# Performance work log

Measured on AMD Instinct MI355X. Metric: run time of the kernel, lower is better.

Reference implementation:

```python
import jax, jax.numpy as jnp
import numpy as np

N_QUBITS = 10
DEPTH = 5
NUM_CLASSES = 2
DIM = 2 ** N_QUBITS  # 1024


def _rx(t):
    # RX(t) = [[cos(t/2), -i sin(t/2)], [-i sin(t/2), cos(t/2)]]
    c, s = jnp.cos(t / 2), jnp.sin(t / 2)
    zr = jnp.zeros_like(t)
    a = jax.lax.complex(c, zr)
    b = jax.lax.complex(zr, -s)
    return jnp.stack([jnp.stack([a, b]), jnp.stack([b, a])]).astype(jnp.complex64)


def _rz(t):
    # RZ(t) = diag(e^{-it/2}, e^{it/2})
    c, s = jnp.cos(t / 2), jnp.sin(t / 2)
    e = jax.lax.complex(c, -s)
    z = jnp.zeros_like(e)
    return jnp.stack([jnp.stack([e, z]), jnp.stack([z, jnp.conj(e)])]).astype(jnp.complex64)


def _apply_1q(state, U, wire):
    # state: (B, 2, ..., 2); wire axis is wire+1 (wire 0 = most significant bit)
    s = jnp.moveaxis(state, wire + 1, -1)
    s = s @ U.T
    return jnp.moveaxis(s, -1, wire + 1)


def _apply_c1q(state, U, ctrl, tgt):
    # controlled-U: apply U on tgt where ctrl qubit is |1>
    s = jnp.moveaxis(state, ctrl + 1, 1)  # (B, 2_ctrl, rest...)
    ax = tgt + 1 if tgt < ctrl else tgt   # tgt axis inside s[:, k]
    s1 = s[:, 1]
    s1 = jnp.moveaxis(s1, ax, -1) @ U.T
    s1 = jnp.moveaxis(s1, -1, ax)
    s = jnp.stack([s[:, 0], s1], axis=1)
    return jnp.moveaxis(s, 1, ctrl + 1)


def _circuit(x, weights, weights_1, weights_2):
    B = x.shape[0]
    x = x.reshape(B, -1)
    x = jnp.pad(x, ((0, 0), (0, DIM - x.shape[1])))  # pad_with=0
    x = x / jnp.linalg.norm(x, axis=1, keepdims=True)  # normalize=True
    state = jax.lax.complex(x, jnp.zeros_like(x)).reshape((B,) + (2,) * N_QUBITS)
    for d in range(DEPTH):
        for i in range(N_QUBITS):
            state = _apply_1q(state, _rx(weights[d, i, 0]), i)
            state = _apply_1q(state, _rz(weights[d, i, 1]), i)
            state = _apply_1q(state, _rx(weights[d, i, 2]), i)
        r = 1 if d % 2 == 0 else 3  # alternating entangler range (CCQC)
        for i in range(N_QUBITS):
            c = (i + r) % N_QUBITS
            state = _apply_c1q(state, _rz(weights[d, i, 3]), c, i)
            state = _apply_c1q(state, _rx(weights[d, i, 4]), c, i)
        state = _apply_1q(state, _rx(weights_1[d]), 0)
        state = _apply_1q(state, _rz(weights_2[d]), 0)
    probs = (jnp.abs(state) ** 2).reshape(B, DIM)
    # <Z_w> signs: bit w (MSB-first) of each basis index
    bits = (jnp.arange(DIM)[None, :] >> (N_QUBITS - 1 - jnp.arange(N_QUBITS)[:, None])) & 1
    zsign = (1 - 2 * bits).astype(probs.dtype)  # (n_qubits, DIM)
    return probs @ zsign.T  # (B, n_qubits)


def setup_inputs() -> dict:
    key = jax.random.key(0)
    ks = jax.random.split(key, 5)
    B = 8192
    x = jax.random.normal(ks[0], (B, 784), dtype=jnp.float32)
    y = jax.random.randint(ks[1], (B,), 0, NUM_CLASSES)
    weights = jax.random.uniform(ks[2], (DEPTH, N_QUBITS, 5), jnp.float32, 0.0, 2 * np.pi)
    weights_1 = jax.random.uniform(ks[3], (DEPTH,), jnp.float32, 0.0, 2 * np.pi)
    weights_2 = jax.random.uniform(ks[4], (DEPTH,), jnp.float32, 0.0, 2 * np.pi)
    return {"x": x, "y": y, "weights": weights, "weights_1": weights_1, "weights_2": weights_2}


def reference(x, y, weights, weights_1, weights_2):
    expz = _circuit(x, weights, weights_1, weights_2)
    logits = expz[:, :NUM_CLASSES]
    logp = jax.nn.log_softmax(logits, axis=-1)
    nll = -jnp.take_along_axis(logp, y[:, None].astype(jnp.int32), axis=1)[:, 0]
    return jnp.mean(nll)  # CrossEntropyLoss (mean reduction)
```

## Files before the change

kernel.cpp:

```cpp
#include <hip/hip_runtime.h>


namespace {

typedef float f32x2 __attribute__((ext_vector_type(2)));
typedef __fp16 fp16x2 __attribute__((ext_vector_type(2)));
typedef _Float16 f16x8 __attribute__((ext_vector_type(8)));
typedef float f32x4v __attribute__((ext_vector_type(4)));

__device__ __forceinline__ f32x2 pk_mul(f32x2 a, f32x2 b) {
  f32x2 d;
  asm("v_pk_mul_f32 %0, %1, %2" : "=v"(d) : "v"(a), "v"(b));
  return d;
}
__device__ __forceinline__ f32x2 pk_fma(f32x2 a, f32x2 b, f32x2 c) {
  f32x2 d;
  asm("v_pk_fma_f32 %0, %1, %2, %3" : "=v"(d) : "v"(a), "v"(b), "v"(c));
  return d;
}
__device__ __forceinline__ f32x2 pk_fma_swap1(f32x2 a, f32x2 b, f32x2 c) {
  f32x2 d;
  asm("v_pk_fma_f32 %0, %1, %2, %3 op_sel:[0,1,0] op_sel_hi:[1,0,1]"
      : "=v"(d) : "v"(a), "v"(b), "v"(c));
  return d;
}
__device__ __forceinline__ f32x2 cmulp(f32x2 cr2, f32x2 ci2, f32x2 v) {
  return pk_fma_swap1(ci2, v, pk_mul(cr2, v));
}
__device__ __forceinline__ f32x2 cmad(f32x2 acc, f32x2 cr2, f32x2 ci2, f32x2 v) {
  return pk_fma_swap1(ci2, v, pk_fma(cr2, v, acc));
}

__device__ __forceinline__ f32x2 shfl_xor2(f32x2 v, int lm) {
  f32x2 r;
  r.x = __shfl_xor(v.x, lm, 64);
  r.y = __shfl_xor(v.y, lm, 64);
  return r;
}
template <int CTRL>
__device__ __forceinline__ f32x2 dpp_xor2(f32x2 v) {
  f32x2 r;
  const int ix = __builtin_bit_cast(int, v.x);
  const int iy = __builtin_bit_cast(int, v.y);
  r.x = __builtin_bit_cast(float,
      __builtin_amdgcn_update_dpp(0, ix, CTRL, 0xF, 0xF, true));
  r.y = __builtin_bit_cast(float,
      __builtin_amdgcn_update_dpp(0, iy, CTRL, 0xF, 0xF, true));
  return r;
}
__device__ __forceinline__ f32x2 shfl_fast(f32x2 v, const int lm) {
  if (lm == 1) return dpp_xor2<0xB1>(v);
  if (lm == 2) return dpp_xor2<0x4E>(v);
  return shfl_xor2(v, lm);
}

struct c2 { float r, i; };
struct m2c { c2 a00, a01, a10, a11; };

__device__ __forceinline__ c2 cmul(c2 x, c2 y) { return {x.r*y.r - x.i*y.i, x.r*y.i + x.i*y.r}; }
__device__ __forceinline__ c2 cadd(c2 x, c2 y) { return {x.r + y.r, x.i + y.i}; }
__device__ __forceinline__ c2 conjc(c2 a) { return {a.r, -a.i}; }
__device__ __forceinline__ m2c mmul(m2c A, m2c B) {
  m2c C;
  C.a00 = cadd(cmul(A.a00, B.a00), cmul(A.a01, B.a10));
  C.a01 = cadd(cmul(A.a00, B.a01), cmul(A.a01, B.a11));
  C.a10 = cadd(cmul(A.a10, B.a00), cmul(A.a11, B.a10));
  C.a11 = cadd(cmul(A.a10, B.a01), cmul(A.a11, B.a11));
  return C;
}
__device__ __forceinline__ m2c madj(m2c U) {
  return { conjc(U.a00), conjc(U.a10), conjc(U.a01), conjc(U.a11) };
}
__device__ __forceinline__ m2c mrx(float t) {
  float c = cosf(0.5f * t), s = sinf(0.5f * t);
  return { {c, 0.f}, {0.f, -s}, {0.f, -s}, {c, 0.f} };
}
__device__ __forceinline__ m2c mrz(float t) {
  float c = cosf(0.5f * t), s = sinf(0.5f * t);
  return { {c, -s}, {0.f, 0.f}, {0.f, 0.f}, {c, s} };
}

__device__ __forceinline__ bool fusable(int d, int i) {
  return (d & 1) ? (i >= 3) : (i >= 1);
}

__global__ void make_prog(const float* __restrict__ w, const float* __restrict__ w1,
                          const float* __restrict__ w2, float* __restrict__ prog) {
  const int t = threadIdx.x;
  int kind = -1, od = 0, oi = 0, p = 0;
  for (int dd = 0; dd < 5; ++dd) {
    const int d = 4 - dd;
    if (d == 4) { if (p == t) kind = 0; ++p; }
    for (int ii = 0; ii < 10; ++ii) {
      const int i = 9 - ii;
      if (p == t) { kind = (d <= 3 && fusable(d, i)) ? 2 : 1; od = d; oi = i; }
      ++p;
    }
    for (int ii = 0; ii < 10; ++ii) {
      const int i = 9 - ii;
      if (d >= 1 && fusable(d - 1, i)) continue;
      if (p == t) { kind = 3; od = d; oi = i; }
      ++p;
    }
  }
  if (kind < 0) return;

  auto u1mat = [&](int d, int i) -> m2c {
    const float* pw = w + (d * 10 + i) * 5;
    m2c U = mmul(mrx(pw[2]), mmul(mrz(pw[1]), mrx(pw[0])));
    if (i == 0 && d > 0) {
      m2c U0 = mmul(mrz(w2[d - 1]), mrx(w1[d - 1]));
      U = mmul(U, U0);
    }
    return U;
  };
  auto cumat = [&](int d, int i) -> m2c {
    const float* pw = w + (d * 10 + i) * 5;
    return mmul(mrx(pw[4]), mrz(pw[3]));
  };

  m2c M0{}, M1{};
  int bt = 9;
  if (kind == 0) {
    M0 = madj(mmul(mrz(w2[4]), mrx(w1[4]))); M1 = M0; bt = 9;
  } else if (kind == 1) {
    M1 = madj(cumat(od, oi));
    M0 = m2c{ {1.f, 0.f}, {0.f, 0.f}, {0.f, 0.f}, {1.f, 0.f} };
    bt = 9 - oi;
  } else if (kind == 2) {
    m2c V1 = madj(u1mat(od + 1, oi));
    m2c VC = madj(cumat(od, oi));
    M0 = V1; M1 = mmul(VC, V1);
    bt = 9 - oi;
  } else {
    M0 = madj(u1mat(od, oi)); M1 = M0; bt = 9 - oi;
  }

  float* o = prog + t * 64;
  if (bt >= 8 || bt < 6) {
    #pragma unroll
    for (int v = 0; v < 4; ++v) {
      const bool hi = (v & 1) != 0;
      const m2c& M = (v >> 1) ? M1 : M0;
      const c2 cA = hi ? M.a11 : M.a00;
      const c2 cB = hi ? M.a10 : M.a01;
      o[v*8+0] = cA.r; o[v*8+1] = cA.r; o[v*8+2] = -cA.i; o[v*8+3] = cA.i;
      o[v*8+4] = cB.r; o[v*8+5] = cB.r; o[v*8+6] = -cB.i; o[v*8+7] = cB.i;
    }
  } else {
    const m2c* Ms[2] = {&M0, &M1};
    #pragma unroll
    for (int c = 0; c < 2; ++c) {
      const c2 e[4] = {Ms[c]->a00, Ms[c]->a01, Ms[c]->a10, Ms[c]->a11};
      #pragma unroll
      for (int q = 0; q < 4; ++q) {
        o[c*16 + q*4 + 0] = e[q].r; o[c*16 + q*4 + 1] = e[q].r;
        o[c*16 + q*4 + 2] = -e[q].i; o[c*16 + q*4 + 3] = e[q].i;
      }
    }
  }
}

struct CoefP { f32x2 Ar, Ai, Br, Bi; };
__device__ __forceinline__ CoefP ldcoef(const float* __restrict__ g, int v) {
  const float4* p = reinterpret_cast<const float4*>(g + v * 8);
  const float4 a = p[0], b = p[1];
  return { f32x2{a.x, a.y}, f32x2{a.z, a.w}, f32x2{b.x, b.y}, f32x2{b.z, b.w} };
}
struct MatP { f32x2 u00r, u00i, u01r, u01i, u10r, u10i, u11r, u11i; };
__device__ __forceinline__ MatP ldmat16(const float* __restrict__ g, int c) {
  const float4* p = reinterpret_cast<const float4*>(g + c * 16);
  const float4 a = p[0], b = p[1], cc = p[2], d = p[3];
  MatP m;
  m.u00r = f32x2{a.x, a.y};  m.u00i = f32x2{a.z, a.w};
  m.u01r = f32x2{b.x, b.y};  m.u01i = f32x2{b.z, b.w};
  m.u10r = f32x2{cc.x, cc.y}; m.u10i = f32x2{cc.z, cc.w};
  m.u11r = f32x2{d.x, d.y};  m.u11i = f32x2{d.z, d.w};
  return m;
}
__device__ __forceinline__ f32x2 capply(const CoefP& c, f32x2 own, f32x2 par) {
  return cmad(cmulp(c.Ar, c.Ai, own), c.Br, c.Bi, par);
}
__device__ __forceinline__ void mat_pair(const MatP& m, f32x2& a, f32x2& b) {
  const f32x2 na = cmad(cmulp(m.u00r, m.u00i, a), m.u01r, m.u01i, b);
  const f32x2 nb = cmad(cmulp(m.u10r, m.u10i, a), m.u11r, m.u11i, b);
  a = na; b = nb;
}

__device__ __forceinline__ void apply_op(f32x2 (&sA)[4], f32x2 (&sB)[4],
                                         f32x2* lxb, const int wv,
                                         const int lane, const float* __restrict__ g,
                                         const int bt, const int bc) {
  if (bt >= 8) {
    const int tb = bt - 8;
    const int hi = (wv >> tb) & 1;
    #pragma unroll
    for (int k = 0; k < 4; ++k) {
      lxb[(wv * 4 + k) * 64 + lane] = sA[k];
      lxb[1024 + (wv * 4 + k) * 64 + lane] = sB[k];
    }
    __syncthreads();
    const int pw = wv ^ (1 << tb);
    f32x2 pA[4], pB[4];
    #pragma unroll
    for (int k = 0; k < 4; ++k) {
      pA[k] = lxb[(pw * 4 + k) * 64 + lane];
      pB[k] = lxb[1024 + (pw * 4 + k) * 64 + lane];
    }
    if (bc >= 8) {
      const int c = (wv >> (bc - 8)) & 1;
      const CoefP cf = ldcoef(g, hi + 2 * c);
      #pragma unroll
      for (int k = 0; k < 4; ++k) {
        sA[k] = capply(cf, sA[k], pA[k]);
        sB[k] = capply(cf, sB[k], pB[k]);
      }
    } else if (bc >= 6) {
      const int cb = bc - 6;
      const CoefP c0 = ldcoef(g, hi), c1 = ldcoef(g, hi + 2);
      #pragma unroll
      for (int k = 0; k < 4; ++k) {
        const CoefP& cf = ((k >> cb) & 1) ? c1 : c0;
        sA[k] = capply(cf, sA[k], pA[k]);
        sB[k] = capply(cf, sB[k], pB[k]);
      }
    } else if (bc >= 0) {
      const int c = (lane >> bc) & 1;
      const CoefP cf = ldcoef(g, hi + 2 * c);
      #pragma unroll
      for (int k = 0; k < 4; ++k) {
        sA[k] = capply(cf, sA[k], pA[k]);
        sB[k] = capply(cf, sB[k], pB[k]);
      }
    } else {
      const CoefP cf = ldcoef(g, hi);
      #pragma unroll
      for (int k = 0; k < 4; ++k) {
        sA[k] = capply(cf, sA[k], pA[k]);
        sB[k] = capply(cf, sB[k], pB[k]);
      }
    }
  } else if (bt >= 6) {
    const int tm = 1 << (bt - 6);
    if (bc >= 6 && bc < 8) {
      const int cb = bc - 6;
      const MatP m0 = ldmat16(g, 0), m1 = ldmat16(g, 1);
      #pragma unroll
      for (int k0 = 0; k0 < 4; ++k0) {
        if (k0 & tm) continue;
        const int k1 = k0 | tm;
        const MatP& m = ((k0 >> cb) & 1) ? m1 : m0;
        mat_pair(m, sA[k0], sA[k1]);
        mat_pair(m, sB[k0], sB[k1]);
      }
    } else {
      int c = 0;
      if (bc >= 8)      c = (wv >> (bc - 8)) & 1;
      else if (bc >= 0) c = (lane >> bc) & 1;
      const MatP m = ldmat16(g, c);
      #pragma unroll
      for (int k0 = 0; k0 < 4; ++k0) {
        if (k0 & tm) continue;
        const int k1 = k0 | tm;
        mat_pair(m, sA[k0], sA[k1]);
        mat_pair(m, sB[k0], sB[k1]);
      }
    }
  } else {
    const int lm = 1 << bt;
    const int hi = (lane >> bt) & 1;
    if (bc >= 6 && bc < 8) {
      const int cb = bc - 6;
      const CoefP c0 = ldcoef(g, hi), c1 = ldcoef(g, hi + 2);
      #pragma unroll
      for (int k = 0; k < 4; ++k) {
        const CoefP& cf = ((k >> cb) & 1) ? c1 : c0;
        const f32x2 pA = shfl_fast(sA[k], lm);
        const f32x2 pB = shfl_fast(sB[k], lm);
        sA[k] = capply(cf, sA[k], pA);
        sB[k] = capply(cf, sB[k], pB);
      }
    } else {
      int c = 1;
      if (bc >= 8)      c = (wv >> (bc - 8)) & 1;
      else if (bc >= 0) c = (lane >> bc) & 1;
      const CoefP cf = ldcoef(g, (bc >= 0) ? (hi + 2 * c) : hi);
      #pragma unroll
      for (int k = 0; k < 4; ++k) {
        const f32x2 pA = shfl_fast(sA[k], lm);
        const f32x2 pB = shfl_fast(sB[k], lm);
        sA[k] = capply(cf, sA[k], pA);
        sB[k] = capply(cf, sB[k], pB);
      }
    }
  }
}

__global__ __launch_bounds__(256) void qprep(const float* __restrict__ prog,
                                             const float* __restrict__ x,
                                             _Float16* __restrict__ Wt,
                                             _Float16* __restrict__ Xh) {
  const int tid = threadIdx.x;
  if (blockIdx.x >= 512) {
    const int t = (blockIdx.x - 512) * 256 + tid;
    const int b = t >> 7;
    const int j = (t & 127) * 8;
    if (j >= 832) return;
    union { fp16x2 h2[4]; f16x8 h8; } u;
    if (j < 784) {
      const float4* p = reinterpret_cast<const float4*>(x + (size_t)b * 784 + j);
      const float4 v0 = p[0], v1 = p[1];
      u.h2[0] = __builtin_amdgcn_cvt_pkrtz(v0.x, v0.y);
      u.h2[1] = __builtin_amdgcn_cvt_pkrtz(v0.z, v0.w);
      u.h2[2] = __builtin_amdgcn_cvt_pkrtz(v1.x, v1.y);
      u.h2[3] = __builtin_amdgcn_cvt_pkrtz(v1.z, v1.w);
    } else {
      #pragma unroll
      for (int q = 0; q < 4; ++q) u.h2[q] = __builtin_amdgcn_cvt_pkrtz(0.f, 0.f);
    }
    *reinterpret_cast<f16x8*>(Xh + (size_t)b * 1024 + j) = u.h8;
    return;
  }

  __shared__ f32x2 lx[2][2048];

  const int lane = tid & 63;
  const int wv = tid >> 6;
  const int n0 = blockIdx.x * 2;
  const int n1 = n0 + 1;

  f32x2 sA[4], sB[4];
  #pragma unroll
  for (int k = 0; k < 4; ++k) {
    const int j = (wv << 8) | (k << 6) | lane;
    sA[k].x = (j == n0) ? 1.f : 0.f; sA[k].y = 0.f;
    sB[k].x = (j == n1) ? 1.f : 0.f; sB[k].y = 0.f;
  }

  int p = 0, ph = 0;
  #pragma unroll
  for (int dd = 0; dd < 5; ++dd) {
    const int d = 4 - dd;
    if (d == 4) {
      apply_op(sA, sB, &lx[ph & 1][0], wv, lane, prog + p * 64, 9, -1);
      ++p; ++ph;
    }
    const int r = (d & 1) ? 3 : 1;
    #pragma unroll
    for (int ii = 0; ii < 10; ++ii) {
      const int i = 9 - ii;
      const int c = (i + r) % 10;
      const int bt = 9 - i, bc = 9 - c;
      apply_op(sA, sB, &lx[ph & 1][0], wv, lane, prog + p * 64, bt, bc);
      ++p; if (bt >= 8) ++ph;
    }
    #pragma unroll
    for (int ii = 0; ii < 10; ++ii) {
      const int i = 9 - ii;
      if (d >= 1 && fusable(d - 1, i)) continue;
      const int bt = 9 - i;
      apply_op(sA, sB, &lx[ph & 1][0], wv, lane, prog + p * 64, bt, -1);
      ++p; if (bt >= 8) ++ph;
    }
  }

  #pragma unroll
  for (int k = 0; k < 4; ++k) {
    const int j = (wv << 8) | (k << 6) | lane;
    Wt[(size_t)(2 * n0) * 1024 + j] = (_Float16)sA[k].x;
    Wt[(size_t)(2 * n0 + 1) * 1024 + j] = (_Float16)(-sA[k].y);
    Wt[(size_t)(2 * n1) * 1024 + j] = (_Float16)sB[k].x;
    Wt[(size_t)(2 * n1 + 1) * 1024 + j] = (_Float16)(-sB[k].y);
  }
}

#define GZ_NSTEP 13

__device__ __forceinline__ void stage_tiles(const _Float16* __restrict__ gA,
                                            const _Float16* __restrict__ gB,
                                            _Float16* sA, _Float16* sB,
                                            int k0, int wv, int lane) {
  const int rIn = lane >> 3;
  const int colh = ((lane & 7) ^ rIn) * 8;
  #pragma unroll
  for (int c = 0; c < 2; ++c) {
    const int chunk = wv * 2 + c;
    const size_t grow = (size_t)(chunk * 8 + rIn) * 1024 + k0 + colh;
    auto* la = (__attribute__((address_space(3))) void*)(sA + chunk * 512 + lane * 8);
    __builtin_amdgcn_global_load_lds(
        (const __attribute__((address_space(1))) void*)(gA + grow), la, 16, 0, 0);
    auto* lb = (__attribute__((address_space(3))) void*)(sB + chunk * 512 + lane * 8);
    __builtin_amdgcn_global_load_lds(
        (const __attribute__((address_space(1))) void*)(gB + grow), lb, 16, 0, 0);
  }
}

__device__ __forceinline__ int lds_off(int row, int slot) {
  return row * 64 + ((slot ^ (row & 7)) * 8);
}

__global__ __launch_bounds__(512) void gemm_z(const _Float16* __restrict__ Xh,
                                              const _Float16* __restrict__ Wt,
                                              float* __restrict__ part, int B) {
  __shared__ _Float16 smA[2][128 * 64];
  __shared__ _Float16 smB[2][128 * 64];

  const int tid = threadIdx.x;
  const int lane = tid & 63;
  const int wv = tid >> 6;
  const int wm = wv >> 1;
  const int wn = wv & 1;
  const int row0 = blockIdx.x * 128;
  const int n0 = blockIdx.y * 128;

  const _Float16* gA = Xh + (size_t)row0 * 1024;
  const _Float16* gB = Wt + (size_t)n0 * 1024;

  const int lr = lane & 15;
  const int lq = lane >> 4;

  f32x4v acc[2][4];
  #pragma unroll
  for (int m = 0; m < 2; ++m)
    #pragma unroll
    for (int f = 0; f < 4; ++f) acc[m][f] = f32x4v{0.f, 0.f, 0.f, 0.f};

  stage_tiles(gA, gB, smA[0], smB[0], 0, wv, lane);
  __syncthreads();

  for (int t = 0; t < GZ_NSTEP; ++t) {
    const int cur = t & 1;
    if (t + 1 < GZ_NSTEP)
      stage_tiles(gA, gB, smA[cur ^ 1], smB[cur ^ 1], (t + 1) * 64, wv, lane);

    #pragma unroll
    for (int kk = 0; kk < 2; ++kk) {
      const int slot = kk * 4 + lq;
      f16x8 a[2], b[4];
      #pragma unroll
      for (int m = 0; m < 2; ++m) {
        const int row = wm * 32 + m * 16 + lr;
        a[m] = *reinterpret_cast<const f16x8*>(&smA[cur][lds_off(row, slot)]);
      }
      #pragma unroll
      for (int f = 0; f < 4; ++f) {
        const int row = wn * 64 + f * 16 + lr;
        b[f] = *reinterpret_cast<const f16x8*>(&smB[cur][lds_off(row, slot)]);
      }
      #pragma unroll
      for (int m = 0; m < 2; ++m)
        #pragma unroll
        for (int f = 0; f < 4; ++f)
          acc[m][f] = __builtin_amdgcn_mfma_f32_16x16x32_f16(a[m], b[f], acc[m][f], 0, 0, 0);
    }
    __syncthreads();
  }

  const int pp = blockIdx.y * 2 + wn;
  #pragma unroll
  for (int m = 0; m < 2; ++m) {
    f32x4v p = f32x4v{0.f, 0.f, 0.f, 0.f};
    #pragma unroll
    for (int f = 0; f < 4; ++f) p += acc[m][f] * acc[m][f];
    #pragma unroll
    for (int msk = 1; msk < 16; msk <<= 1) {
      p.x += __shfl_xor(p.x, msk, 64);
      p.y += __shfl_xor(p.y, msk, 64);
      p.z += __shfl_xor(p.z, msk, 64);
      p.w += __shfl_xor(p.w, msk, 64);
    }
    if (lr == 0) {
      const int rbase = row0 + wm * 32 + m * 16 + lq * 4;
      float* dst = part + (size_t)pp * B + rbase;
      dst[0] = p.x; dst[1] = p.y; dst[2] = p.z; dst[3] = p.w;
    }
  }
}

__global__ __launch_bounds__(256) void nll_part(const float* __restrict__ part,
                                                const int* __restrict__ y,
                                                float* __restrict__ out2, int B) {
  const int row = blockIdx.x * 256 + threadIdx.x;
  float q0 = 0.f, q1 = 0.f, nn = 0.f;
  #pragma unroll
  for (int pp = 0; pp < 32; ++pp) {
    const float P = part[(size_t)pp * B + row];
    q0 += (pp & 16) ? -P : P;
    q1 += (pp & 8) ? -P : P;
    nn += P;
  }
  const float z0 = q0 / nn, z1 = q1 / nn;
  const float mx = fmaxf(z0, z1);
  const float lse = mx + logf(expf(z0 - mx) + expf(z1 - mx));
  const float ly = (y[row] == 0) ? z0 : z1;
  float s = lse - ly;
  #pragma unroll
  for (int msk = 1; msk < 64; msk <<= 1) s += __shfl_xor(s, msk, 64);
  __shared__ float red[4];
  if ((threadIdx.x & 63) == 0) red[threadIdx.x >> 6] = s;
  __syncthreads();
  if (threadIdx.x == 0) out2[blockIdx.x] = red[0] + red[1] + red[2] + red[3];
}

__global__ void nll_final(const float* __restrict__ out2, float* __restrict__ out,
                          int nblk, float scale) {
  const int t = threadIdx.x;
  float s = (t < nblk) ? out2[t] : 0.f;
  #pragma unroll
  for (int msk = 1; msk < 64; msk <<= 1) s += __shfl_xor(s, msk, 64);
  if (t == 0) out[0] = s * scale;
}

}

extern "C" void kernel_launch(void* const* d_in, const int* in_sizes, int n_in,
                              void* d_out, int out_size, void* d_ws, size_t ws_size,
                              hipStream_t stream) {
  const float* x  = (const float*)d_in[0];
  const int*   y  = (const int*)d_in[1];
  const float* w  = (const float*)d_in[2];
  const float* w1 = (const float*)d_in[3];
  const float* w2 = (const float*)d_in[4];
  float* out = (float*)d_out;

  const int B = in_sizes[0] / 784;

  char* ws = (char*)d_ws;
  _Float16* Wt   = (_Float16*)ws;
  _Float16* Xh   = (_Float16*)(ws + (size_t)2048 * 1024 * 2);
  float*    part = (float*)(ws + (size_t)2048 * 1024 * 2 + (size_t)B * 1024 * 2);
  float*    out2 = part + (size_t)32 * B;
  float*    prog = out2 + 64;

  make_prog<<<1, 128, 0, stream>>>(w, w1, w2, prog);
  qprep<<<512 + (B * 128) / 256, 256, 0, stream>>>(prog, x, Wt, Xh);
  gemm_z<<<dim3(B / 128, 16), 512, 0, stream>>>(Xh, Wt, part, B);
  nll_part<<<B / 256, 256, 0, stream>>>(part, y, out2, B);
  nll_final<<<1, 64, 0, stream>>>(out2, out, B / 256, 1.0f / (float)B);
}
```

Measured before the change: 78.26 us.

## Remap amplitude index bits to waves and fold final reduction into atomics

Reorders the in-block state layout so the per-thread register index holds the top two qubit bits and the wave index holds bits 6-7. The two most-significant qubits, which the circuit touches most often including the per-layer qubit-0 gates, are then applied in registers with no LDS exchange or barrier, and the LDS round-trip moves to bits 6-7. It also drops the nll_final launch: nll_part accumulates scaled block sums into the output with atomicAdd, and make_prog zeroes the output first. This removes one kernel launch but makes the float summation order nondeterministic.

```diff
diff --git a/kernel.cpp b/kernel.cpp
--- a/kernel.cpp
+++ b/kernel.cpp
@@ -85,8 +85,10 @@
 }
 
 __global__ void make_prog(const float* __restrict__ w, const float* __restrict__ w1,
-                          const float* __restrict__ w2, float* __restrict__ prog) {
+                          const float* __restrict__ w2, float* __restrict__ prog,
+                          float* __restrict__ outp) {
   const int t = threadIdx.x;
+  if (t == 127) outp[0] = 0.f;
   int kind = -1, od = 0, oi = 0, p = 0;
   for (int dd = 0; dd < 5; ++dd) {
     const int d = 4 - dd;
@@ -137,7 +139,18 @@
   }
 
   float* o = prog + t * 64;
-  if (bt >= 8 || bt < 6) {
+  if (bt >= 8) {
+    const m2c* Ms[2] = {&M0, &M1};
+    #pragma unroll
+    for (int c = 0; c < 2; ++c) {
+      const c2 e[4] = {Ms[c]->a00, Ms[c]->a01, Ms[c]->a10, Ms[c]->a11};
+      #pragma unroll
+      for (int q = 0; q < 4; ++q) {
+        o[c*16 + q*4 + 0] = e[q].r; o[c*16 + q*4 + 1] = e[q].r;
+        o[c*16 + q*4 + 2] = -e[q].i; o[c*16 + q*4 + 3] = e[q].i;
+      }
+    }
+  } else {
     #pragma unroll
     for (int v = 0; v < 4; ++v) {
       const bool hi = (v & 1) != 0;
@@ -146,17 +159,6 @@
       const c2 cB = hi ? M.a10 : M.a01;
       o[v*8+0] = cA.r; o[v*8+1] = cA.r; o[v*8+2] = -cA.i; o[v*8+3] = cA.i;
       o[v*8+4] = cB.r; o[v*8+5] = cB.r; o[v*8+6] = -cB.i; o[v*8+7] = cB.i;
-    }
-  } else {
-    const m2c* Ms[2] = {&M0, &M1};
-    #pragma unroll
-    for (int c = 0; c < 2; ++c) {
-      const c2 e[4] = {Ms[c]->a00, Ms[c]->a01, Ms[c]->a10, Ms[c]->a11};
-      #pragma unroll
-      for (int q = 0; q < 4; ++q) {
-        o[c*16 + q*4 + 0] = e[q].r; o[c*16 + q*4 + 1] = e[q].r;
-        o[c*16 + q*4 + 2] = -e[q].i; o[c*16 + q*4 + 3] = e[q].i;
-      }
     }
   }
 }
@@ -192,58 +194,9 @@
                                          const int lane, const float* __restrict__ g,
                                          const int bt, const int bc) {
   if (bt >= 8) {
-    const int tb = bt - 8;
-    const int hi = (wv >> tb) & 1;
-    #pragma unroll
-    for (int k = 0; k < 4; ++k) {
-      lxb[(wv * 4 + k) * 64 + lane] = sA[k];
-      lxb[1024 + (wv * 4 + k) * 64 + lane] = sB[k];
-    }
-    __syncthreads();
-    const int pw = wv ^ (1 << tb);
-    f32x2 pA[4], pB[4];
-    #pragma unroll
-    for (int k = 0; k < 4; ++k) {
-      pA[k] = lxb[(pw * 4 + k) * 64 + lane];
-      pB[k] = lxb[1024 + (pw * 4 + k) * 64 + lane];
-    }
+    const int tm = 1 << (bt - 8);
     if (bc >= 8) {
-      const int c = (wv >> (bc - 8)) & 1;
-      const CoefP cf = ldcoef(g, hi + 2 * c);
-      #pragma unroll
-      for (int k = 0; k < 4; ++k) {
-        sA[k] = capply(cf, sA[k], pA[k]);
-        sB[k] = capply(cf, sB[k], pB[k]);
-      }
-    } else if (bc >= 6) {
-      const int cb = bc - 6;
-      const CoefP c0 = ldcoef(g, hi), c1 = ldcoef(g, hi + 2);
-      #pragma unroll
-      for (int k = 0; k < 4; ++k) {
-        const CoefP& cf = ((k >> cb) & 1) ? c1 : c0;
-        sA[k] = capply(cf, sA[k], pA[k]);
-        sB[k] = capply(cf, sB[k], pB[k]);
-      }
-    } else if (bc >= 0) {
-      const int c = (lane >> bc) & 1;
-      const CoefP cf = ldcoef(g, hi + 2 * c);
-      #pragma unroll
-      for (int k = 0; k < 4; ++k) {
-        sA[k] = capply(cf, sA[k], pA[k]);
-        sB[k] = capply(cf, sB[k], pB[k]);
-      }
-    } else {
-      const CoefP cf = ldcoef(g, hi);
-      #pragma unroll
-      for (int k = 0; k < 4; ++k) {
-        sA[k] = capply(cf, sA[k], pA[k]);
-        sB[k] = capply(cf, sB[k], pB[k]);
-      }
-    }
-  } else if (bt >= 6) {
-    const int tm = 1 << (bt - 6);
-    if (bc >= 6 && bc < 8) {
-      const int cb = bc - 6;
+      const int cb = bc - 8;
       const MatP m0 = ldmat16(g, 0), m1 = ldmat16(g, 1);
       #pragma unroll
       for (int k0 = 0; k0 < 4; ++k0) {
@@ -255,7 +208,7 @@
       }
     } else {
       int c = 0;
-      if (bc >= 8)      c = (wv >> (bc - 8)) & 1;
+      if (bc >= 6)      c = (wv >> (bc - 6)) & 1;
       else if (bc >= 0) c = (lane >> bc) & 1;
       const MatP m = ldmat16(g, c);
       #pragma unroll
@@ -266,11 +219,47 @@
         mat_pair(m, sB[k0], sB[k1]);
       }
     }
+  } else if (bt >= 6) {
+    const int tb = bt - 6;
+    const int hi = (wv >> tb) & 1;
+    #pragma unroll
+    for (int k = 0; k < 4; ++k) {
+      lxb[(wv * 4 + k) * 64 + lane] = sA[k];
+      lxb[1024 + (wv * 4 + k) * 64 + lane] = sB[k];
+    }
+    __syncthreads();
+    const int pw = wv ^ (1 << tb);
+    f32x2 pA[4], pB[4];
+    #pragma unroll
+    for (int k = 0; k < 4; ++k) {
+      pA[k] = lxb[(pw * 4 + k) * 64 + lane];
+      pB[k] = lxb[1024 + (pw * 4 + k) * 64 + lane];
+    }
+    if (bc >= 8) {
+      const int cb = bc - 8;
+      const CoefP c0 = ldcoef(g, hi), c1 = ldcoef(g, hi + 2);
+      #pragma unroll
+      for (int k = 0; k < 4; ++k) {
+        const CoefP& cf = ((k >> cb) & 1) ? c1 : c0;
+        sA[k] = capply(cf, sA[k], pA[k]);
+        sB[k] = capply(cf, sB[k], pB[k]);
+      }
+    } else {
+      int c = 0;
+      if (bc >= 6)      c = (wv >> (bc - 6)) & 1;
+      else if (bc >= 0) c = (lane >> bc) & 1;
+      const CoefP cf = ldcoef(g, hi + 2 * c);
+      #pragma unroll
+      for (int k = 0; k < 4; ++k) {
+        sA[k] = capply(cf, sA[k], pA[k]);
+        sB[k] = capply(cf, sB[k], pB[k]);
+      }
+    }
   } else {
     const int lm = 1 << bt;
     const int hi = (lane >> bt) & 1;
-    if (bc >= 6 && bc < 8) {
-      const int cb = bc - 6;
+    if (bc >= 8) {
+      const int cb = bc - 8;
       const CoefP c0 = ldcoef(g, hi), c1 = ldcoef(g, hi + 2);
       #pragma unroll
       for (int k = 0; k < 4; ++k) {
@@ -281,10 +270,10 @@
         sB[k] = capply(cf, sB[k], pB);
       }
     } else {
-      int c = 1;
-      if (bc >= 8)      c = (wv >> (bc - 8)) & 1;
+      int c = 0;
+      if (bc >= 6)      c = (wv >> (bc - 6)) & 1;
       else if (bc >= 0) c = (lane >> bc) & 1;
-      const CoefP cf = ldcoef(g, (bc >= 0) ? (hi + 2 * c) : hi);
+      const CoefP cf = ldcoef(g, hi + 2 * c);
       #pragma unroll
       for (int k = 0; k < 4; ++k) {
         const f32x2 pA = shfl_fast(sA[k], lm);
@@ -332,7 +321,7 @@
   f32x2 sA[4], sB[4];
   #pragma unroll
   for (int k = 0; k < 4; ++k) {
-    const int j = (wv << 8) | (k << 6) | lane;
+    const int j = (k << 8) | (wv << 6) | lane;
     sA[k].x = (j == n0) ? 1.f : 0.f; sA[k].y = 0.f;
     sB[k].x = (j == n1) ? 1.f : 0.f; sB[k].y = 0.f;
   }
@@ -343,7 +332,7 @@
     const int d = 4 - dd;
     if (d == 4) {
       apply_op(sA, sB, &lx[ph & 1][0], wv, lane, prog + p * 64, 9, -1);
-      ++p; ++ph;
+      ++p;
     }
     const int r = (d & 1) ? 3 : 1;
     #pragma unroll
@@ -352,7 +341,7 @@
       const int c = (i + r) % 10;
       const int bt = 9 - i, bc = 9 - c;
       apply_op(sA, sB, &lx[ph & 1][0], wv, lane, prog + p * 64, bt, bc);
-      ++p; if (bt >= 8) ++ph;
+      ++p; if (bt >= 6 && bt < 8) ++ph;
     }
     #pragma unroll
     for (int ii = 0; ii < 10; ++ii) {
@@ -360,13 +349,13 @@
       if (d >= 1 && fusable(d - 1, i)) continue;
       const int bt = 9 - i;
       apply_op(sA, sB, &lx[ph & 1][0], wv, lane, prog + p * 64, bt, -1);
-      ++p; if (bt >= 8) ++ph;
+      ++p; if (bt >= 6 && bt < 8) ++ph;
     }
   }
 
   #pragma unroll
   for (int k = 0; k < 4; ++k) {
-    const int j = (wv << 8) | (k << 6) | lane;
+    const int j = (k << 8) | (wv << 6) | lane;
     Wt[(size_t)(2 * n0) * 1024 + j] = (_Float16)sA[k].x;
     Wt[(size_t)(2 * n0 + 1) * 1024 + j] = (_Float16)(-sA[k].y);
     Wt[(size_t)(2 * n1) * 1024 + j] = (_Float16)sB[k].x;
@@ -479,7 +468,8 @@
 
 __global__ __launch_bounds__(256) void nll_part(const float* __restrict__ part,
                                                 const int* __restrict__ y,
-                                                float* __restrict__ out2, int B) {
+                                                float* __restrict__ out, int B,
+                                                float scale) {
   const int row = blockIdx.x * 256 + threadIdx.x;
   float q0 = 0.f, q1 = 0.f, nn = 0.f;
   #pragma unroll
@@ -499,16 +489,8 @@
   __shared__ float red[4];
   if ((threadIdx.x & 63) == 0) red[threadIdx.x >> 6] = s;
   __syncthreads();
-  if (threadIdx.x == 0) out2[blockIdx.x] = red[0] + red[1] + red[2] + red[3];
-}
-
-__global__ void nll_final(const float* __restrict__ out2, float* __restrict__ out,
-                          int nblk, float scale) {
-  const int t = threadIdx.x;
-  float s = (t < nblk) ? out2[t] : 0.f;
-  #pragma unroll
-  for (int msk = 1; msk < 64; msk <<= 1) s += __shfl_xor(s, msk, 64);
-  if (t == 0) out[0] = s * scale;
+  if (threadIdx.x == 0)
+    atomicAdd(out, (red[0] + red[1] + red[2] + red[3]) * scale);
 }
 
 }
@@ -529,12 +511,10 @@
   _Float16* Wt   = (_Float16*)ws;
   _Float16* Xh   = (_Float16*)(ws + (size_t)2048 * 1024 * 2);
   float*    part = (float*)(ws + (size_t)2048 * 1024 * 2 + (size_t)B * 1024 * 2);
-  float*    out2 = part + (size_t)32 * B;
-  float*    prog = out2 + 64;
-
-  make_prog<<<1, 128, 0, stream>>>(w, w1, w2, prog);
+  float*    prog = part + (size_t)32 * B;
+
+  make_prog<<<1, 128, 0, stream>>>(w, w1, w2, prog, out);
   qprep<<<512 + (B * 128) / 256, 256, 0, stream>>>(prog, x, Wt, Xh);
   gemm_z<<<dim3(B / 128, 16), 512, 0, stream>>>(Xh, Wt, part, B);
-  nll_part<<<B / 256, 256, 0, stream>>>(part, y, out2, B);
-  nll_final<<<1, 64, 0, stream>>>(out2, out, B / 256, 1.0f / (float)B);
-}
+  nll_part<<<B / 256, 256, 0, stream>>>(part, y, out, B, 1.0f / (float)B);
+}
```

Result: faster. 75.37 us (-3.7%).
